# Kernel optimization log

Measured on AMD Instinct MI355X. Metric: run time of the kernel, lower is better.

The kernel has to match this reference:

```python
import jax, jax.numpy as jnp
import numpy as np

LUMINANCE_Q = np.array([
    [16, 11, 10, 16, 24, 40, 51, 61],
    [12, 12, 14, 19, 26, 58, 60, 55],
    [14, 13, 16, 24, 40, 57, 69, 56],
    [14, 17, 22, 29, 51, 87, 80, 62],
    [18, 22, 37, 56, 68, 109, 103, 77],
    [24, 36, 55, 64, 81, 104, 113, 92],
    [49, 64, 78, 87, 103, 121, 120, 101],
    [72, 92, 95, 98, 112, 100, 103, 99]], dtype=np.float64) / 100.0

def _dct_matrix():
    # C[k, n] = grid_factors[k] * cos(pi*k*(2n+1)/16); grid_factors = 2*[1/sqrt(32), 1/sqrt(16)x7]
    k = np.arange(8)[:, None]
    n = np.arange(8)[None, :]
    a = np.full(8, 2.0 / np.sqrt(2 * 8))
    a[0] = 2.0 / np.sqrt(4 * 8)
    C = a[:, None] * np.cos(np.pi * k * (2 * n + 1) / 16.0)
    return jnp.asarray(C, dtype=jnp.float32)

DCT_C = _dct_matrix()
Q_TABLE = jnp.asarray(LUMINANCE_Q, dtype=jnp.float32)

def setup_inputs() -> dict:
    key = jax.random.key(0)
    k1, k2 = jax.random.split(key)
    B, H, W = 16, 1024, 1024
    # pixel-like values around 128
    image = 128.0 + 40.0 * jax.random.normal(k1, (B, 1, H, W), dtype=jnp.float32)
    quality_factor = jax.random.randint(k2, (B,), 1, 100).astype(jnp.float32)
    return {"image": image, "quality_factor": quality_factor}

def reference(image, quality_factor):
    B, _, H, W = image.shape
    # Set_QF: factor per batch element, shape [B,1,1,1,1]
    factor = jnp.where(quality_factor < 50.0,
                       5000.0 / quality_factor,
                       200.0 - 2.0 * quality_factor).reshape(B, 1, 1, 1, 1)
    # Image_2_Blocks: [B, H/8, 8, W/8, 8] -> [B, 8, 8, H/8, W/8], then center
    blocks = image.reshape(B, H // 8, 8, W // 8, 8).transpose(0, 2, 4, 1, 3) - 128.0
    # 2D orthonormal DCT-II over the two 8-wide in-block axes (axes 1 then 2)
    dct = jnp.einsum('un,vm,bnmij->buvij', DCT_C, DCT_C, blocks)
    out = dct / (factor * Q_TABLE[None, :, :, None, None])
    # quantize=False: no rounding
    return out.reshape(B, 64, H // 8, W // 8)
```

## Files before the change

### kernel.cpp

```cpp
#include <hip/hip_runtime.h>
#include <cstddef>


static constexpr double LUMQ[64] = {
    16, 11, 10, 16, 24, 40, 51, 61,
    12, 12, 14, 19, 26, 58, 60, 55,
    14, 13, 16, 24, 40, 57, 69, 56,
    14, 17, 22, 29, 51, 87, 80, 62,
    18, 22, 37, 56, 68, 109, 103, 77,
    24, 36, 55, 64, 81, 104, 113, 92,
    49, 64, 78, 87, 103, 121, 120, 101,
    72, 92, 95, 98, 112, 100, 103, 99,
};

static constexpr double AANS[8] = {
    1.0, 1.3870398453221475, 1.3065629648763766, 1.1758756024193588,
    1.0, 0.7856949583871022, 0.5411961001461970, 0.2758993792829430,
};

__device__ __host__ __forceinline__ constexpr float outScale(int u, int v) {
    return (float)(100.0 / (LUMQ[u * 8 + v] * 8.0 * AANS[u] * AANS[v]));
}

__device__ __forceinline__ void aan_dct8(float& x0, float& x1, float& x2,
                                         float& x3, float& x4, float& x5,
                                         float& x6, float& x7) {
    const float t0 = x0 + x7, t7 = x0 - x7;
    const float t1 = x1 + x6, t6 = x1 - x6;
    const float t2 = x2 + x5, t5 = x2 - x5;
    const float t3 = x3 + x4, t4 = x3 - x4;

    float t10 = t0 + t3;
    const float t13 = t0 - t3;
    const float t11 = t1 + t2;
    const float t12 = t1 - t2;
    x0 = t10 + t11;
    x4 = t10 - t11;
    const float z1 = (t12 + t13) * 0.70710678118654752f;
    x2 = t13 + z1;
    x6 = t13 - z1;

    t10 = t4 + t5;
    const float u11 = t5 + t6;
    const float u12 = t6 + t7;
    const float z5 = (t10 - u12) * 0.38268343236508977f;
    const float z2 = 0.54119610014619698f * t10 + z5;
    const float z4 = 1.30656296487637653f * u12 + z5;
    const float z3 = u11 * 0.70710678118654752f;
    const float z11 = t7 + z3;
    const float z13 = t7 - z3;
    x5 = z13 + z2;
    x3 = z13 - z2;
    x1 = z11 + z4;
    x7 = z11 - z4;
}

__global__ __launch_bounds__(256) void jpeg_dct_quant_kernel(
    const float* __restrict__ img,
    const float* __restrict__ qfv,
    float* __restrict__ out)
{
    const int bid = blockIdx.x * 256 + threadIdx.x;
    const int j = bid & 127;
    const int i = (bid >> 7) & 127;
    const int b = bid >> 14;

    const float* src = img + ((size_t)b << 20) + (size_t)(i * 8) * 1024 + j * 8;

    float m[8][8];
    #pragma unroll
    for (int n = 0; n < 8; ++n) {
        const float4 r0 = *reinterpret_cast<const float4*>(src + (size_t)n * 1024);
        const float4 r1 = *reinterpret_cast<const float4*>(src + (size_t)n * 1024 + 4);
        m[n][0] = r0.x; m[n][1] = r0.y; m[n][2] = r0.z; m[n][3] = r0.w;
        m[n][4] = r1.x; m[n][5] = r1.y; m[n][6] = r1.z; m[n][7] = r1.w;
    }

    #pragma unroll
    for (int n = 0; n < 8; ++n)
        aan_dct8(m[n][0], m[n][1], m[n][2], m[n][3],
                 m[n][4], m[n][5], m[n][6], m[n][7]);

    #pragma unroll
    for (int v = 0; v < 8; ++v)
        aan_dct8(m[0][v], m[1][v], m[2][v], m[3][v],
                 m[4][v], m[5][v], m[6][v], m[7][v]);

    m[0][0] -= 8192.0f;

    const float qf = qfv[b];
    const float factor = (qf < 50.0f) ? (5000.0f / qf) : (200.0f - 2.0f * qf);
    const float invf = 1.0f / factor;

    float* dst = out + ((size_t)b << 20) + (size_t)i * 128 + j;
    #pragma unroll
    for (int u = 0; u < 8; ++u)
        #pragma unroll
        for (int v = 0; v < 8; ++v)
            dst[(size_t)(u * 8 + v) * 16384] = m[u][v] * (invf * outScale(u, v));
}

extern "C" void kernel_launch(void* const* d_in, const int* in_sizes, int n_in,
                              void* d_out, int out_size, void* d_ws, size_t ws_size,
                              hipStream_t stream) {
    const float* img = (const float*)d_in[0];
    const float* qfv = (const float*)d_in[1];
    float* out = (float*)d_out;

    jpeg_dct_quant_kernel<<<1024, 256, 0, stream>>>(img, qfv, out);
}
```

Measured before the change: 111.5 us.

## Stage image strips through LDS and split output rows across thread pairs

Each workgroup now loads a full 8-row strip with contiguous float4 reads into padded shared memory, then each 8x8 block is transformed by two threads that each write half of the frequency rows. The grid doubles to increase parallelism and shorten per-thread store chains. The DCT is computed redundantly twice per block. The padded LDS stride may produce misaligned vector LDS reads.

```diff
diff --git a/kernel.cpp b/kernel.cpp
--- a/kernel.cpp
+++ b/kernel.cpp
@@ -55,32 +55,50 @@
     x7 = z11 - z4;
 }
 
+#define BLK_STRIDE 65
+
 __global__ __launch_bounds__(256) void jpeg_dct_quant_kernel(
     const float* __restrict__ img,
     const float* __restrict__ qfv,
     float* __restrict__ out)
 {
-    const int bid = blockIdx.x * 256 + threadIdx.x;
-    const int j = bid & 127;
-    const int i = (bid >> 7) & 127;
-    const int b = bid >> 14;
+    __shared__ float sm[BLK_STRIDE * 128];
 
-    const float* src = img + ((size_t)b << 20) + (size_t)(i * 8) * 1024 + j * 8;
+    const int t   = threadIdx.x;
+    const int row = blockIdx.x;
+    const int b   = row >> 7;
+    const int i   = row & 127;
+
+    const float* strip = img + ((size_t)b << 20) + (size_t)(i * 8) * 1024;
+    const int wj = t >> 1;
+    const int wm = (t & 1) * 4;
+    #pragma unroll
+    for (int p = 0; p < 8; ++p) {
+        const float4 r =
+            *reinterpret_cast<const float4*>(strip + (size_t)p * 1024 + 4 * t);
+        float* d = &sm[wj * BLK_STRIDE + p * 8 + wm];
+        d[0] = r.x; d[1] = r.y; d[2] = r.z; d[3] = r.w;
+    }
+
+    __syncthreads();
+
+    const int jb   = t & 127;
+    const int half = t >> 7;
+    const float* blk = &sm[jb * BLK_STRIDE];
 
     float m[8][8];
     #pragma unroll
     for (int n = 0; n < 8; ++n) {
-        const float4 r0 = *reinterpret_cast<const float4*>(src + (size_t)n * 1024);
-        const float4 r1 = *reinterpret_cast<const float4*>(src + (size_t)n * 1024 + 4);
-        m[n][0] = r0.x; m[n][1] = r0.y; m[n][2] = r0.z; m[n][3] = r0.w;
-        m[n][4] = r1.x; m[n][5] = r1.y; m[n][6] = r1.z; m[n][7] = r1.w;
+        const float4 lo = *reinterpret_cast<const float4*>(blk + n * 8);
+        const float4 hi = *reinterpret_cast<const float4*>(blk + n * 8 + 4);
+        m[n][0] = lo.x; m[n][1] = lo.y; m[n][2] = lo.z; m[n][3] = lo.w;
+        m[n][4] = hi.x; m[n][5] = hi.y; m[n][6] = hi.z; m[n][7] = hi.w;
     }
 
     #pragma unroll
     for (int n = 0; n < 8; ++n)
         aan_dct8(m[n][0], m[n][1], m[n][2], m[n][3],
                  m[n][4], m[n][5], m[n][6], m[n][7]);
-
     #pragma unroll
     for (int v = 0; v < 8; ++v)
         aan_dct8(m[0][v], m[1][v], m[2][v], m[3][v],
@@ -92,12 +110,15 @@
     const float factor = (qf < 50.0f) ? (5000.0f / qf) : (200.0f - 2.0f * qf);
     const float invf = 1.0f / factor;
 
-    float* dst = out + ((size_t)b << 20) + (size_t)i * 128 + j;
+    float* dst = out + ((size_t)b << 20) + (size_t)i * 128 + jb;
+    const int u0 = half * 4;
     #pragma unroll
-    for (int u = 0; u < 8; ++u)
+    for (int uu = 0; uu < 4; ++uu) {
+        const int u = u0 + uu;
         #pragma unroll
         for (int v = 0; v < 8; ++v)
             dst[(size_t)(u * 8 + v) * 16384] = m[u][v] * (invf * outScale(u, v));
+    }
 }
 
 extern "C" void kernel_launch(void* const* d_in, const int* in_sizes, int n_in,
@@ -107,5 +128,5 @@
     const float* qfv = (const float*)d_in[1];
     float* out = (float*)d_out;
 
-    jpeg_dct_quant_kernel<<<1024, 256, 0, stream>>>(img, qfv, out);
+    jpeg_dct_quant_kernel<<<2048, 256, 0, stream>>>(img, qfv, out);
 }
```

New measurement: 173.8 us. 1.56x slower.
